# Performance work log

Hardware: AMD Instinct MI355X
Metric: run time of the kernel (lower is better)

The kernel has to match this reference:

```python
import jax, jax.numpy as jnp
import numpy as np

N, B, C, K, H = 65536, 4, 512, 256, 8


def setup_inputs() -> dict:
    key = jax.random.key(0)
    ks = jax.random.split(key, 6)
    feat = jax.random.normal(ks[0], (N, C), dtype=jnp.float32)
    cls_tokens = jax.random.normal(ks[1], (B, C), dtype=jnp.float32)
    Wqkv = jax.random.normal(ks[2], (C, 3 * C), dtype=jnp.float32) * 0.02
    bqkv = jnp.zeros((3 * C,), dtype=jnp.float32)
    Wproj = jax.random.normal(ks[3], (C, C), dtype=jnp.float32) * 0.02
    bproj = jnp.zeros((C,), dtype=jnp.float32)
    order = jax.random.permutation(ks[4], N)          # serialized order (permutation)
    inverse = jnp.argsort(order)                       # its inverse
    offset = jnp.arange(1, B + 1) * (N // B)           # equal-size point clouds, divisible by K
    return {"feat": feat, "cls_tokens": cls_tokens, "Wqkv": Wqkv, "bqkv": bqkv,
            "Wproj": Wproj, "bproj": bproj, "order": order, "inverse": inverse,
            "offset": offset, "patch_size": K, "num_heads": H}


def reference(feat, cls_tokens, Wqkv, bqkv, Wproj, bproj, order, inverse, offset, patch_size, num_heads):
    n, c = feat.shape
    b = offset.shape[0]
    k = patch_size
    h = num_heads
    dh = c // h
    scale = dh ** -0.5
    n_chunks = n // k

    # qkv projection, gather into serialized order
    qkv = (feat @ Wqkv + bqkv)[order]                  # [N, 3C]
    cls_qkv = cls_tokens @ Wqkv + bqkv                 # [B, 3C]

    # chunk -> batch assignment (offsets are chunk-aligned here)
    chunk_starts = jnp.arange(n_chunks) * k
    batch_id = jnp.searchsorted(offset, chunk_starts, side="right")  # [n_chunks]
    acc = jax.nn.one_hot(batch_id, b, dtype=feat.dtype)              # [n_chunks, B]
    agg = acc.T / acc.T.sum(axis=1, keepdims=True)                   # [B, n_chunks]

    cls_per_chunk = acc @ cls_qkv                                    # [n_chunks, 3C]
    qkv_c = qkv.reshape(n_chunks, k, 3 * c)
    qkv_c = jnp.concatenate([cls_per_chunk[:, None, :], qkv_c], axis=1)  # [n_chunks, K+1, 3C]

    qkv_c = qkv_c.reshape(n_chunks, k + 1, 3, h, dh)
    q = qkv_c[:, :, 0].transpose(0, 2, 1, 3)           # [n_chunks, H, K+1, dh]
    kk = qkv_c[:, :, 1].transpose(0, 2, 1, 3)
    v = qkv_c[:, :, 2].transpose(0, 2, 1, 3)

    # upcast_attention / upcast_softmax = True
    attn = jnp.einsum("nhqd,nhkd->nhqk", q.astype(jnp.float32) * scale, kk.astype(jnp.float32))
    attn = jax.nn.softmax(attn, axis=-1).astype(feat.dtype)
    out = jnp.einsum("nhqk,nhkd->nhqd", attn, v)       # [n_chunks, H, K+1, dh]
    out = out.transpose(0, 2, 1, 3).reshape(n_chunks, k + 1, c)

    feat_out = out[:, 1:, :].reshape(-1, c)[inverse]   # scatter back to original order
    feat_out = feat_out @ Wproj + bproj                # proj (proj_drop is identity in eval)
    cls_feat = agg @ out[:, 0, :]                      # [B, C] (no proj, per source)
    return feat_out, cls_feat
```

## Files before the change

### kernel.cpp

```cpp
#include <hip/hip_runtime.h>


typedef float  floatx4 __attribute__((ext_vector_type(4)));
typedef __bf16 bf16x8  __attribute__((ext_vector_type(8)));

__device__ __forceinline__ __bf16 f2bf(float x) {
  unsigned u = __builtin_bit_cast(unsigned, x);
  u = u + 0x7FFFu + ((u >> 16) & 1u);
  unsigned short h = (unsigned short)(u >> 16);
  return __builtin_bit_cast(__bf16, h);
}

__device__ __forceinline__ floatx4 mfma_16x16x32(bf16x8 a, bf16x8 b, floatx4 c) {
  return __builtin_amdgcn_mfma_f32_16x16x32_bf16(a, b, c, 0, 0, 0);
}

__device__ __forceinline__ void gload16(const void* g, void* l) {
  __builtin_amdgcn_global_load_lds(
      (const __attribute__((address_space(1))) unsigned int*)g,
      (__attribute__((address_space(3))) unsigned int*)l, 16, 0, 0);
}

__global__ void cast_gather_feat(const float* __restrict__ feat,
                                 const int* __restrict__ order,
                                 __bf16* __restrict__ dst) {
  long i = ((long)blockIdx.x * blockDim.x + threadIdx.x) * 8;
  int row = (int)(i >> 9);
  int col = (int)(i & 511);
  const float* sp = feat + (long)order[row] * 512 + col;
  float4 a = *(const float4*)sp;
  float4 b = *(const float4*)(sp + 4);
  bf16x8 o;
  o[0] = f2bf(a.x); o[1] = f2bf(a.y); o[2] = f2bf(a.z); o[3] = f2bf(a.w);
  o[4] = f2bf(b.x); o[5] = f2bf(b.y); o[6] = f2bf(b.z); o[7] = f2bf(b.w);
  *(bf16x8*)(dst + i) = o;
}

__global__ void transpose_cast(const float* __restrict__ W, __bf16* __restrict__ Wt,
                               int K, int N) {
  __shared__ float tile[32][33];
  const int n0 = blockIdx.x * 32, k0 = blockIdx.y * 32;
  const int c = threadIdx.x & 31, r8 = threadIdx.x >> 5;
#pragma unroll
  for (int i = 0; i < 4; ++i) {
    int r = r8 + i * 8;
    tile[r][c] = W[(long)(k0 + r) * N + n0 + c];
  }
  __syncthreads();
#pragma unroll
  for (int i = 0; i < 4; ++i) {
    int r = r8 + i * 8;
    Wt[(long)(n0 + r) * K + k0 + c] = f2bf(tile[c][r]);
  }
}

__global__ void cls_qkv_kernel(const float* __restrict__ cls_tokens,
                               const float* __restrict__ Wqkv,
                               const float* __restrict__ bqkv,
                               __bf16* __restrict__ clsqkv, int N3) {
  __shared__ float red[256];
  const int c = threadIdx.x & 63, part = threadIdx.x >> 6;
  const int o = blockIdx.x * 64 + c;
  const int b = o / N3, n = o - b * N3;
  float sv = 0.f;
  const int kst = part * 128;
  for (int k = kst; k < kst + 128; ++k)
    sv += cls_tokens[b * 512 + k] * Wqkv[(long)k * N3 + n];
  red[threadIdx.x] = sv;
  __syncthreads();
  if (part == 0)
    clsqkv[o] = f2bf(red[c] + red[c + 64] + red[c + 128] + red[c + 192] + bqkv[n]);
}

template <int OUT_F32>
__global__ __launch_bounds__(256, 2) void gemm_bt(
    const __bf16* __restrict__ A, const __bf16* __restrict__ Bt,
    const float* __restrict__ bias, void* __restrict__ C,
    int N, int K) {
  __shared__ __align__(16) __bf16 As[128 * 64];
  __shared__ __align__(16) __bf16 Bs[128 * 64];
  const int tid = threadIdx.x;
  const int wave = tid >> 6, lane = tid & 63;
  const int quad = lane >> 4, l15 = lane & 15;
  const int wr = wave >> 1, wc = wave & 1;
  const long m0 = (long)blockIdx.x * 128;
  const int n0 = blockIdx.y * 128;
  const int srow8 = lane >> 3;
  const int sc8p = lane & 7;

  floatx4 zero = {0.f, 0.f, 0.f, 0.f};
  floatx4 acc[4][4];
#pragma unroll
  for (int i = 0; i < 4; ++i)
#pragma unroll
    for (int j = 0; j < 4; ++j) acc[i][j] = zero;

  for (int kt = 0; kt < K; kt += 64) {
    __syncthreads();
#pragma unroll
    for (int i = 0; i < 4; ++i) {
      const int rbase = i * 32 + wave * 8;
      const int row = rbase + srow8;
      const int c8 = sc8p ^ (row & 7);
      gload16(A + (m0 + row) * K + kt + c8 * 8, As + rbase * 64);
      gload16(Bt + (long)(n0 + row) * K + kt + c8 * 8, Bs + rbase * 64);
    }
    __syncthreads();
#pragma unroll
    for (int ks = 0; ks < 2; ++ks) {
      bf16x8 af[4], bfr[4];
#pragma unroll
      for (int mi = 0; mi < 4; ++mi) {
        int row = wr * 64 + mi * 16 + l15;
        int c8 = ks * 4 + quad;
        af[mi] = *(const bf16x8*)(As + row * 64 + ((c8 ^ (row & 7)) << 3));
      }
#pragma unroll
      for (int ni = 0; ni < 4; ++ni) {
        int row = wc * 64 + ni * 16 + l15;
        int c8 = ks * 4 + quad;
        bfr[ni] = *(const bf16x8*)(Bs + row * 64 + ((c8 ^ (row & 7)) << 3));
      }
#pragma unroll
      for (int mi = 0; mi < 4; ++mi)
#pragma unroll
        for (int ni = 0; ni < 4; ++ni)
          acc[mi][ni] = mfma_16x16x32(af[mi], bfr[ni], acc[mi][ni]);
    }
  }
#pragma unroll
  for (int mi = 0; mi < 4; ++mi) {
#pragma unroll
    for (int ni = 0; ni < 4; ++ni) {
      const int col = n0 + wc * 64 + ni * 16 + l15;
      const float bb = bias[col];
#pragma unroll
      for (int r = 0; r < 4; ++r) {
        const long row = m0 + wr * 64 + mi * 16 + quad * 4 + r;
        float v = acc[mi][ni][r] + bb;
        if (OUT_F32)
          ((float*)C)[row * N + col] = v;
        else
          ((__bf16*)C)[row * N + col] = f2bf(v);
      }
    }
  }
}

__global__ __launch_bounds__(256, 4) void attn_kernel(
    const __bf16* __restrict__ qkv,
    const __bf16* __restrict__ clsqkv,
    const int* __restrict__ order,
    const int* __restrict__ offset,
    __bf16* __restrict__ outO,
    float* __restrict__ outcls,
    int B) {
  __shared__ __align__(16) __bf16 Vt[64 * 264];
  __shared__ __align__(16) __bf16 Pbuf[4 * 16 * 40];
  __shared__ unsigned ktab[272];
  const int chunk = blockIdx.x & 255;
  const int h = blockIdx.x >> 8;
  const int tid = threadIdx.x;
  const int wave = tid >> 6, lane = tid & 63;
  const int quad = lane >> 4, l15 = lane & 15;
  const int cs = chunk << 8;
  int batch = 0;
  for (int b = 0; b < B; ++b) batch += (offset[b] <= cs) ? 1 : 0;
  const unsigned clsoff =
      (unsigned)((const char*)(clsqkv + (long)batch * 1536) - (const char*)qkv);

  for (int t = tid; t < 272; t += 256)
    ktab[t] = (t == 0) ? clsoff : (unsigned)(cs + ((t <= 256) ? t : 256) - 1) * 3072u;

  const int qoffB = h * 128;
  const int koffB = 1024 + h * 128;
  const int voffB = 2048 + h * 128;

  {
    const int rsub = lane >> 3, c8 = lane & 7;
#pragma unroll
    for (int p = 0; p < 8; ++p) {
      int t = p * 32 + wave * 8 + rsub;
      unsigned ro = (t == 0) ? clsoff : (unsigned)(cs + t - 1) * 3072u;
      bf16x8 v = *(const bf16x8*)((const char*)qkv + ro + voffB + c8 * 16);
#pragma unroll
      for (int j = 0; j < 8; ++j) Vt[(c8 * 8 + j) * 264 + t] = v[j];
    }
    if (tid < 8) {
      bf16x8 v = *(const bf16x8*)((const char*)qkv +
                                  (unsigned)(cs + 255) * 3072u + voffB + tid * 16);
#pragma unroll
      for (int j = 0; j < 8; ++j) Vt[(tid * 8 + j) * 264 + 256] = v[j];
    }
  }
  __syncthreads();

  float v256[4];
#pragma unroll
  for (int ni = 0; ni < 4; ++ni) v256[ni] = (float)Vt[(ni * 16 + l15) * 264 + 256];
  __bf16* Pw = Pbuf + wave * (16 * 40);

  for (int rt = wave; rt < 17; rt += 4) {
    const unsigned qo = ktab[rt * 16 + l15];
    bf16x8 qf0 = *(const bf16x8*)((const char*)qkv + qo + qoffB + quad * 16);
    bf16x8 qf1 = *(const bf16x8*)((const char*)qkv + qo + qoffB + 64 + quad * 16);

    floatx4 zero = {0.f, 0.f, 0.f, 0.f};
    floatx4 s[17];
#pragma unroll
    for (int i = 0; i < 17; ++i) s[i] = zero;
#pragma unroll
    for (int k2 = 0; k2 < 17; ++k2) {
      const unsigned ko = ktab[k2 * 16 + l15];
      bf16x8 kf0 = *(const bf16x8*)((const char*)qkv + ko + koffB + quad * 16);
      bf16x8 kf1 = *(const bf16x8*)((const char*)qkv + ko + koffB + 64 + quad * 16);
      s[k2] = mfma_16x16x32(qf0, kf0, s[k2]);
      s[k2] = mfma_16x16x32(qf1, kf1, s[k2]);
    }

    float mx[4] = {-3.0e38f, -3.0e38f, -3.0e38f, -3.0e38f};
#pragma unroll
    for (int k2 = 0; k2 < 16; ++k2)
#pragma unroll
      for (int r = 0; r < 4; ++r) mx[r] = fmaxf(mx[r], s[k2][r]);
#pragma unroll
    for (int r = 0; r < 4; ++r) {
      float v = (l15 == 0) ? s[16][r] : -3.0e38f;
      s[16][r] = v;
      mx[r] = fmaxf(mx[r], v);
    }
#pragma unroll
    for (int off = 1; off < 16; off <<= 1)
#pragma unroll
      for (int r = 0; r < 4; ++r) mx[r] = fmaxf(mx[r], __shfl_xor(mx[r], off, 16));
    const float c1 = 0.125f * 1.44269504f;
    float mb[4], sum[4] = {0.f, 0.f, 0.f, 0.f};
#pragma unroll
    for (int r = 0; r < 4; ++r) mb[r] = mx[r] * c1;
#pragma unroll
    for (int k2 = 0; k2 < 17; ++k2)
#pragma unroll
      for (int r = 0; r < 4; ++r) {
        float e = __builtin_amdgcn_exp2f(fmaf(s[k2][r], c1, -mb[r]));
        s[k2][r] = e;
        sum[r] += e;
      }
#pragma unroll
    for (int off = 1; off < 16; off <<= 1)
#pragma unroll
      for (int r = 0; r < 4; ++r) sum[r] += __shfl_xor(sum[r], off, 16);
    float rl[4];
#pragma unroll
    for (int r = 0; r < 4; ++r) rl[r] = 1.0f / sum[r];

    floatx4 o[4];
#pragma unroll
    for (int i = 0; i < 4; ++i) o[i] = zero;
#pragma unroll
    for (int ks = 0; ks < 8; ++ks) {
#pragma unroll
      for (int half = 0; half < 2; ++half) {
        int kt2 = ks * 2 + half;
#pragma unroll
        for (int r = 0; r < 4; ++r)
          Pw[(quad * 4 + r) * 40 + half * 16 + l15] = f2bf(s[kt2][r]);
      }
      asm volatile("s_waitcnt lgkmcnt(0)" ::: "memory");
      bf16x8 pf = *(const bf16x8*)(Pw + l15 * 40 + quad * 8);
#pragma unroll
      for (int ni = 0; ni < 4; ++ni) {
        bf16x8 vf = *(const bf16x8*)(Vt + (ni * 16 + l15) * 264 + ks * 32 + quad * 8);
        o[ni] = mfma_16x16x32(pf, vf, o[ni]);
      }
    }
    float p256[4];
#pragma unroll
    for (int r = 0; r < 4; ++r) p256[r] = __shfl(s[16][r], lane & 48, 64);
#pragma unroll
    for (int ni = 0; ni < 4; ++ni)
#pragma unroll
      for (int r = 0; r < 4; ++r)
        o[ni][r] = (o[ni][r] + p256[r] * v256[ni]) * rl[r];

#pragma unroll
    for (int r = 0; r < 4; ++r) {
      int q = rt * 16 + quad * 4 + r;
      if (q > 256) continue;
      if (q == 0) {
#pragma unroll
        for (int ni = 0; ni < 4; ++ni)
          outcls[(long)chunk * 512 + h * 64 + ni * 16 + l15] = o[ni][r];
      } else {
        long orow = (long)order[cs + q - 1];
#pragma unroll
        for (int ni = 0; ni < 4; ++ni)
          outO[orow * 512 + h * 64 + ni * 16 + l15] = f2bf(o[ni][r]);
      }
    }
  }
}

__global__ void cls_feat_kernel(const float* __restrict__ outcls,
                                const int* __restrict__ offset,
                                float* __restrict__ dst, int B, int C) {
  int i = blockIdx.x * blockDim.x + threadIdx.x;
  if (i >= B * C) return;
  int b = i / C, c = i - b * C;
  int st = (b == 0) ? 0 : offset[b - 1];
  int en = offset[b];
  int c0 = st >> 8, c1 = en >> 8;
  float s = 0.f;
  for (int ch = c0; ch < c1; ++ch) s += outcls[(long)ch * C + c];
  dst[i] = s / (float)(c1 - c0);
}

extern "C" void kernel_launch(void* const* d_in, const int* in_sizes, int n_in,
                              void* d_out, int out_size, void* d_ws, size_t ws_size,
                              hipStream_t stream) {
  const float* feat       = (const float*)d_in[0];
  const float* cls_tokens = (const float*)d_in[1];
  const float* Wqkv       = (const float*)d_in[2];
  const float* bqkv       = (const float*)d_in[3];
  const float* Wproj      = (const float*)d_in[4];
  const float* bproj      = (const float*)d_in[5];
  const int*   order      = (const int*)d_in[6];
  const int*   offset     = (const int*)d_in[8];
  const int B = in_sizes[8];

  char* ws = (char*)d_ws;
  __bf16* qkv    = (__bf16*)(ws);
  __bf16* featb  = (__bf16*)(ws + 201326592);
  __bf16* outO   = featb;
  __bf16* wqkvT  = (__bf16*)(ws + 268435456);
  __bf16* wprojT = (__bf16*)(ws + 270008320);
  __bf16* clsqkv = (__bf16*)(ws + 270532608);
  float*  outcls = (float*)(ws + 270544896);

  float* feat_out = (float*)d_out;
  float* cls_out  = feat_out + (long)65536 * 512;

  cast_gather_feat<<<16384, 256, 0, stream>>>(feat, order, featb);
  transpose_cast<<<dim3(48, 16), 256, 0, stream>>>(Wqkv, wqkvT, 512, 1536);
  transpose_cast<<<dim3(16, 16), 256, 0, stream>>>(Wproj, wprojT, 512, 512);
  cls_qkv_kernel<<<96, 256, 0, stream>>>(cls_tokens, Wqkv, bqkv, clsqkv, 1536);

  gemm_bt<0><<<dim3(512, 12), 256, 0, stream>>>(featb, wqkvT, bqkv, (void*)qkv, 1536, 512);

  attn_kernel<<<2048, 256, 0, stream>>>(qkv, clsqkv, order, offset, outO, outcls, B);

  gemm_bt<1><<<dim3(512, 4), 256, 0, stream>>>(outO, wprojT, bproj, (void*)feat_out, 512, 512);

  cls_feat_kernel<<<8, 256, 0, stream>>>(outcls, offset, cls_out, B, 512);
}
```

Measured before the change: 688.8 us.

## Stage attention K tile in swizzled LDS, skew V transpose, reorder GEMM grid

Measured after the change: 609.0 us. 1.13x faster.

```diff
diff --git a/kernel.cpp b/kernel.cpp
--- a/kernel.cpp
+++ b/kernel.cpp
@@ -83,8 +83,8 @@
   const int wave = tid >> 6, lane = tid & 63;
   const int quad = lane >> 4, l15 = lane & 15;
   const int wr = wave >> 1, wc = wave & 1;
-  const long m0 = (long)blockIdx.x * 128;
-  const int n0 = blockIdx.y * 128;
+  const long m0 = (long)blockIdx.y * 128;
+  const int n0 = blockIdx.x * 128;
   const int srow8 = lane >> 3;
   const int sc8p = lane & 7;
 
@@ -147,7 +147,7 @@
   }
 }
 
-__global__ __launch_bounds__(256, 4) void attn_kernel(
+__global__ __launch_bounds__(256, 2) void attn_kernel(
     const __bf16* __restrict__ qkv,
     const __bf16* __restrict__ clsqkv,
     const int* __restrict__ order,
@@ -155,9 +155,9 @@
     __bf16* __restrict__ outO,
     float* __restrict__ outcls,
     int B) {
-  __shared__ __align__(16) __bf16 Vt[64 * 264];
+  __shared__ __align__(16) __bf16 Ks[272 * 64];
+  __shared__ __align__(16) __bf16 Vt[64 * 264 + 64];
   __shared__ __align__(16) __bf16 Pbuf[4 * 16 * 40];
-  __shared__ unsigned ktab[272];
   const int chunk = blockIdx.x & 255;
   const int h = blockIdx.x >> 8;
   const int tid = threadIdx.x;
@@ -169,12 +169,23 @@
   const unsigned clsoff =
       (unsigned)((const char*)(clsqkv + (long)batch * 1536) - (const char*)qkv);
 
-  for (int t = tid; t < 272; t += 256)
-    ktab[t] = (t == 0) ? clsoff : (unsigned)(cs + ((t <= 256) ? t : 256) - 1) * 3072u;
-
   const int qoffB = h * 128;
   const int koffB = 1024 + h * 128;
   const int voffB = 2048 + h * 128;
+
+  auto rowoff = [&](int t) -> unsigned {
+    int tt = (t <= 256) ? t : 256;
+    return (tt == 0) ? clsoff : (unsigned)(cs + tt - 1) * 3072u;
+  };
+
+  {
+    const int rsub = lane >> 3, c8 = lane & 7;
+    for (int i = wave; i < 34; i += 4) {
+      int r = i * 8 + rsub;
+      gload16((const char*)qkv + rowoff(r) + koffB + ((c8 ^ (r & 7)) << 4),
+              Ks + i * 512);
+    }
+  }
 
   {
     const int rsub = lane >> 3, c8 = lane & 7;
@@ -184,24 +195,34 @@
       unsigned ro = (t == 0) ? clsoff : (unsigned)(cs + t - 1) * 3072u;
       bf16x8 v = *(const bf16x8*)((const char*)qkv + ro + voffB + c8 * 16);
 #pragma unroll
-      for (int j = 0; j < 8; ++j) Vt[(c8 * 8 + j) * 264 + t] = v[j];
+      for (int j = 0; j < 8; ++j)
+        Vt[(c8 * 8 + j) * 264 + c8 * 8 + t] = v[j];
     }
     if (tid < 8) {
       bf16x8 v = *(const bf16x8*)((const char*)qkv +
                                   (unsigned)(cs + 255) * 3072u + voffB + tid * 16);
 #pragma unroll
-      for (int j = 0; j < 8; ++j) Vt[(tid * 8 + j) * 264 + 256] = v[j];
+      for (int j = 0; j < 8; ++j)
+        Vt[(tid * 8 + j) * 264 + tid * 8 + 256] = v[j];
     }
   }
   __syncthreads();
 
+  int vbase[4];
+#pragma unroll
+  for (int ni = 0; ni < 4; ++ni) {
+    int d = ni * 16 + l15;
+    vbase[ni] = d * 264 + ((ni * 2 + (l15 >> 3)) & 7) * 8;
+  }
   float v256[4];
 #pragma unroll
-  for (int ni = 0; ni < 4; ++ni) v256[ni] = (float)Vt[(ni * 16 + l15) * 264 + 256];
+  for (int ni = 0; ni < 4; ++ni) v256[ni] = (float)Vt[vbase[ni] + 256];
   __bf16* Pw = Pbuf + wave * (16 * 40);
+  const int sw = l15 & 7;
+  const __bf16* kb = Ks + l15 * 64;
 
   for (int rt = wave; rt < 17; rt += 4) {
-    const unsigned qo = ktab[rt * 16 + l15];
+    const unsigned qo = rowoff(rt * 16 + l15);
     bf16x8 qf0 = *(const bf16x8*)((const char*)qkv + qo + qoffB + quad * 16);
     bf16x8 qf1 = *(const bf16x8*)((const char*)qkv + qo + qoffB + 64 + quad * 16);
 
@@ -211,9 +232,9 @@
     for (int i = 0; i < 17; ++i) s[i] = zero;
 #pragma unroll
     for (int k2 = 0; k2 < 17; ++k2) {
-      const unsigned ko = ktab[k2 * 16 + l15];
-      bf16x8 kf0 = *(const bf16x8*)((const char*)qkv + ko + koffB + quad * 16);
-      bf16x8 kf1 = *(const bf16x8*)((const char*)qkv + ko + koffB + 64 + quad * 16);
+      const __bf16* kr = kb + k2 * 1024;
+      bf16x8 kf0 = *(const bf16x8*)(kr + ((quad ^ sw) << 3));
+      bf16x8 kf1 = *(const bf16x8*)(kr + (((quad + 4) ^ sw) << 3));
       s[k2] = mfma_16x16x32(qf0, kf0, s[k2]);
       s[k2] = mfma_16x16x32(qf1, kf1, s[k2]);
     }
@@ -269,7 +290,7 @@
       bf16x8 pf = *(const bf16x8*)(Pw + l15 * 40 + quad * 8);
 #pragma unroll
       for (int ni = 0; ni < 4; ++ni) {
-        bf16x8 vf = *(const bf16x8*)(Vt + (ni * 16 + l15) * 264 + ks * 32 + quad * 8);
+        bf16x8 vf = *(const bf16x8*)(Vt + vbase[ni] + ks * 32 + quad * 8);
         o[ni] = mfma_16x16x32(pf, vf, o[ni]);
       }
     }
@@ -344,11 +365,11 @@
   transpose_cast<<<dim3(16, 16), 256, 0, stream>>>(Wproj, wprojT, 512, 512);
   cls_qkv_kernel<<<96, 256, 0, stream>>>(cls_tokens, Wqkv, bqkv, clsqkv, 1536);
 
-  gemm_bt<0><<<dim3(512, 12), 256, 0, stream>>>(featb, wqkvT, bqkv, (void*)qkv, 1536, 512);
+  gemm_bt<0><<<dim3(12, 512), 256, 0, stream>>>(featb, wqkvT, bqkv, (void*)qkv, 1536, 512);
 
   attn_kernel<<<2048, 256, 0, stream>>>(qkv, clsqkv, order, offset, outO, outcls, B);
 
-  gemm_bt<1><<<dim3(512, 4), 256, 0, stream>>>(outO, wprojT, bproj, (void*)feat_out, 512, 512);
+  gemm_bt<1><<<dim3(4, 512), 256, 0, stream>>>(outO, wprojT, bproj, (void*)feat_out, 512, 512);
 
   cls_feat_kernel<<<8, 256, 0, stream>>>(outcls, offset, cls_out, B, 512);
 }
```
